# Optimization experiments

Measured on AMD Instinct MI355X. Metric: run time of the kernel, lower is better.

The kernel has to match this reference:

```python
import jax, jax.numpy as jnp
import numpy as np

B, D, UNITS = 32768, 1024, 1024
NB_FACTOR, SPARSITY = 3, 32
NB = D // SPARSITY  # 32 blocks of 32x32 per block-diagonal factor


def _block_t_matmul(kb, y):
    # kb: [nb, bi, bo] block-diagonal factor values; y: [nb*bi, batch]
    # computes blockdiag(kb)^T @ y without materializing the dense matrix
    nb, bi, bo = kb.shape
    yb = y.reshape(nb, bi, -1)                      # [nb, bi, batch]
    out = jnp.einsum('nio,nib->nob', kb, yb)        # [nb, bo, batch]
    return out.reshape(nb * bo, -1)


def setup_inputs() -> dict:
    key = jax.random.key(0)
    ks = jax.random.split(key, 9)
    return {
        'x': jax.random.normal(ks[0], (B, D), jnp.float32),
        'P0': jax.random.normal(ks[1], (D, D), jnp.float32),
        'P1': jax.random.normal(ks[2], (D, D), jnp.float32),
        'P2': jax.random.normal(ks[3], (D, D), jnp.float32),
        'P3': jax.random.normal(ks[4], (UNITS, UNITS), jnp.float32),
        'K0': jax.random.normal(ks[5], (NB, SPARSITY, SPARSITY), jnp.float32) * 0.05,
        'K1': jax.random.normal(ks[6], (NB, SPARSITY, SPARSITY), jnp.float32) * 0.05,
        'K2': jax.random.normal(ks[7], (NB, SPARSITY, SPARSITY), jnp.float32) * 0.05,
        'bias': jax.random.normal(ks[8], (UNITS,), jnp.float32),
    }


def reference(x, P0, P1, P2, P3, K0, K1, K2, bias):
    # output = (softmax(P3) @ Bd2^T @ softmax(P2) @ Bd1^T @ softmax(P1) @ Bd0^T @ softmax(P0) @ x^T)^T + bias
    y = x.T                                          # [D, B]
    y = jax.nn.softmax(P0, axis=1) @ y
    for kb, perm in ((K0, P1), (K1, P2), (K2, P3)):
        y = _block_t_matmul(kb, y)
        y = jax.nn.softmax(perm, axis=1) @ y
    out = y.T + bias                                 # [B, UNITS]
    return out
```

## Files before the change

kernel.cpp:

```cpp
#include <hip/hip_runtime.h>
#include <hip/hip_bf16.h>

typedef __bf16 bf16x8 __attribute__((ext_vector_type(8)));
typedef float f32x4 __attribute__((ext_vector_type(4)));
typedef unsigned short u16x8 __attribute__((ext_vector_type(8)));

__device__ __forceinline__ unsigned short f2bf(float f) {
  unsigned u = __float_as_uint(f);
  u += 0x7FFF + ((u >> 16) & 1);
  return (unsigned short)(u >> 16);
}
__device__ __forceinline__ float bf2f(unsigned short h) {
  return __uint_as_float((unsigned)h << 16);
}

__device__ __forceinline__ void gload_lds16(const void* g, void* l) {
  __builtin_amdgcn_global_load_lds(
      (const __attribute__((address_space(1))) void*)g,
      (__attribute__((address_space(3))) void*)l, 16, 0, 0);
}

__device__ __forceinline__ void convert_slice(const float* __restrict__ x,
                                              unsigned short* __restrict__ xb,
                                              int base8, int cnt8, int cb, int nb)
{
  int i = cb * 256 + (int)threadIdx.x;
  const int stride = nb * 256;
  for (; i < cnt8; i += stride) {
    const size_t g = (size_t)(base8 + i);
    float4 v0 = ((const float4*)x)[2 * g];
    float4 v1 = ((const float4*)x)[2 * g + 1];
    u16x8 uv;
    uv[0] = f2bf(v0.x); uv[1] = f2bf(v0.y); uv[2] = f2bf(v0.z); uv[3] = f2bf(v0.w);
    uv[4] = f2bf(v1.x); uv[5] = f2bf(v1.y); uv[6] = f2bf(v1.z); uv[7] = f2bf(v1.w);
    ((u16x8*)xb)[g] = uv;
  }
}

__global__ __launch_bounds__(256)
void softmax4_kernel(const float* __restrict__ P0, const float* __restrict__ P1,
                     const float* __restrict__ P2, const float* __restrict__ P3,
                     unsigned short* __restrict__ S,
                     const float* __restrict__ cvx, unsigned short* __restrict__ cvxb,
                     int cvt_cnt)
{
  if (blockIdx.x >= 4096) {
    convert_slice(cvx, cvxb, 0, cvt_cnt, blockIdx.x - 4096, gridDim.x - 4096);
    return;
  }
  const int bid = blockIdx.x;
  const int mat = bid >> 10, row = bid & 1023;
  const float* P = (mat == 0 ? P0 : mat == 1 ? P1 : mat == 2 ? P2 : P3) + (size_t)row * 1024;
  unsigned short* out = S + ((size_t)mat << 20) + (size_t)row * 1024;
  const int t = threadIdx.x, w = t >> 6, l = t & 63;
  float4 v = ((const float4*)P)[t];
  float mx = fmaxf(fmaxf(v.x, v.y), fmaxf(v.z, v.w));
  #pragma unroll
  for (int off = 32; off > 0; off >>= 1) mx = fmaxf(mx, __shfl_xor(mx, off));
  __shared__ float redA[4], redB[4];
  if (l == 0) redA[w] = mx;
  __syncthreads();
  mx = fmaxf(fmaxf(redA[0], redA[1]), fmaxf(redA[2], redA[3]));
  float e0 = __expf(v.x - mx), e1 = __expf(v.y - mx);
  float e2 = __expf(v.z - mx), e3 = __expf(v.w - mx);
  float s = e0 + e1 + e2 + e3;
  #pragma unroll
  for (int off = 32; off > 0; off >>= 1) s += __shfl_xor(s, off);
  if (l == 0) redB[w] = s;
  __syncthreads();
  s = redB[0] + redB[1] + redB[2] + redB[3];
  float inv = 1.0f / s;
  ushort4 o;
  o.x = f2bf(e0 * inv); o.y = f2bf(e1 * inv);
  o.z = f2bf(e2 * inv); o.w = f2bf(e3 * inv);
  ((ushort4*)out)[t] = o;
}

__device__ __forceinline__ void bdT_body(const float* __restrict__ Kb,
                                         const unsigned short* __restrict__ in,
                                         unsigned short* __restrict__ outT, int bid)
{
  const int n = bid >> 2;
  const int c = (bid & 3) * 256 + threadIdx.x;
  __shared__ float Ks[32][33];
  for (int t = threadIdx.x; t < 1024; t += 256)
    Ks[t >> 5][t & 31] = Kb[n * 1024 + t];
  __syncthreads();
  float ri[32];
  #pragma unroll
  for (int i = 0; i < 32; ++i)
    ri[i] = bf2f(in[(size_t)(n * 32 + i) * 1024 + c]);
  unsigned short ov[32];
  #pragma unroll
  for (int o = 0; o < 32; ++o) {
    float acc = 0.f;
    #pragma unroll
    for (int i = 0; i < 32; ++i) acc = fmaf(Ks[i][o], ri[i], acc);
    ov[o] = f2bf(acc);
  }
  u16x8* dst = (u16x8*)(outT + (size_t)c * 1024 + n * 32);
  const u16x8* src = (const u16x8*)ov;
  #pragma unroll
  for (int q = 0; q < 4; ++q) dst[q] = src[q];
}

__global__ __launch_bounds__(256)
void blockdiagT_dual_kernel(const float* Ka, const unsigned short* ina, unsigned short* outa,
                            const float* Kb2, const unsigned short* inb, unsigned short* outb,
                            const float* cvx, unsigned short* cvxb, int cvt_base, int cvt_cnt)
{
  const int bid = blockIdx.x;
  if (bid >= 256) {
    convert_slice(cvx, cvxb, cvt_base, cvt_cnt, bid - 256, gridDim.x - 256);
    return;
  }
  const bool sec = bid >= 128;
  bdT_body(sec ? Kb2 : Ka, sec ? inb : ina, sec ? outb : outa, sec ? bid - 128 : bid);
}

template<int TILE, bool A_FP32, bool OUT_BIAS, bool RBD>
__device__ __forceinline__ void gemm_body(const void* __restrict__ Av,
                                          const unsigned short* __restrict__ B,
                                          void* __restrict__ Cv, const float* __restrict__ bias,
                                          int N, int K, int nprim, int bid,
                                          const float* __restrict__ KR)
{
  constexpr int FR  = TILE / 32;
  constexpr int SIT = TILE / 32;
  __shared__ unsigned short Asm[TILE * 64];
  __shared__ unsigned short Bsm[TILE * 64];
  const int tid = threadIdx.x;
  const int w = tid >> 6, l = tid & 63;
  const int cpx = nprim >> 3;
  const int swz = (bid & 7) * cpx + (bid >> 3);
  const int ntn = N / TILE;
  const int n0 = (swz % ntn) * TILE;
  const int m0 = (swz / ntn) * TILE;
  const int wr = (w >> 1) * (TILE / 2), wc = (w & 1) * (TILE / 2);
  const int lr = l & 15, kg = (l >> 4) << 3;

  f32x4 acc[FR][FR] = {};
  const int KT = K >> 6;
  for (int kt = 0; kt < KT; ++kt) {
    const int k0 = kt << 6;
    if (kt) __syncthreads();
    #pragma unroll
    for (int it = 0; it < SIT; ++it) {
      int li = it * 256 + tid;
      int row = li >> 3, c8 = (li & 7) << 3;
      const unsigned short* g = B + (size_t)(n0 + row) * K + (k0 + c8);
      gload_lds16(g, (char*)Bsm + it * 4096 + w * 1024);
    }
    if (A_FP32) {
      const float* Af = (const float*)Av;
      #pragma unroll
      for (int p = 0; p < SIT; ++p) {
        int row = (tid >> 3) + p * 32;
        int c8 = (tid & 7) << 3;
        const float* g = Af + (size_t)(m0 + row) * K + (k0 + c8);
        float4 v0 = ((const float4*)g)[0];
        float4 v1 = ((const float4*)g)[1];
        u16x8 uv;
        uv[0] = f2bf(v0.x); uv[1] = f2bf(v0.y); uv[2] = f2bf(v0.z); uv[3] = f2bf(v0.w);
        uv[4] = f2bf(v1.x); uv[5] = f2bf(v1.y); uv[6] = f2bf(v1.z); uv[7] = f2bf(v1.w);
        *(u16x8*)&Asm[row * 64 + c8] = uv;
      }
    } else {
      const unsigned short* Ab = (const unsigned short*)Av;
      #pragma unroll
      for (int it = 0; it < SIT; ++it) {
        int li = it * 256 + tid;
        int row = li >> 3, c8 = (li & 7) << 3;
        const unsigned short* g = Ab + (size_t)(m0 + row) * K + (k0 + c8);
        gload_lds16(g, (char*)Asm + it * 4096 + w * 1024);
      }
    }
    __syncthreads();
    #pragma unroll
    for (int ks = 0; ks < 2; ++ks) {
      const int kb = ks * 32 + kg;
      bf16x8 af[FR], bfr[FR];
      #pragma unroll
      for (int i = 0; i < FR; ++i)
        af[i] = *(const bf16x8*)&Asm[(wr + i * 16 + lr) * 64 + kb];
      #pragma unroll
      for (int j = 0; j < FR; ++j)
        bfr[j] = *(const bf16x8*)&Bsm[(wc + j * 16 + lr) * 64 + kb];
      #pragma unroll
      for (int i = 0; i < FR; ++i)
        #pragma unroll
        for (int j = 0; j < FR; ++j)
          acc[i][j] = __builtin_amdgcn_mfma_f32_16x16x32_bf16(af[i], bfr[j], acc[i][j], 0, 0, 0);
    }
  }
  const int cr = (l >> 4) << 2;
  const int cc = l & 15;
  if (RBD) {
    __shared__ float tileS[64][65];
    __shared__ float Kt[2][32][33];
    __syncthreads();
    #pragma unroll
    for (int j = 0; j < FR; ++j)
      #pragma unroll
      for (int i = 0; i < FR; ++i)
        #pragma unroll
        for (int r = 0; r < 4; ++r)
          tileS[wr + i * 16 + cr + r][wc + j * 16 + cc] = acc[i][j][r];
    for (int idx = tid; idx < 2048; idx += 256) {
      int blk = idx >> 10, rem = idx & 1023;
      Kt[blk][rem >> 5][rem & 31] = KR[(size_t)((n0 >> 5) + blk) * 1024 + rem];
    }
    __syncthreads();
    const int row = tid & 63, cq = (tid >> 6) << 4;
    const int nb2 = cq >> 5, co = cq & 31;
    float av[16] = {};
    #pragma unroll 4
    for (int o = 0; o < 32; ++o) {
      float a = tileS[row][nb2 * 32 + o];
      #pragma unroll
      for (int ii = 0; ii < 16; ++ii)
        av[ii] = fmaf(a, Kt[nb2][o][co + ii], av[ii]);
    }
    u16x8 ov[2];
    #pragma unroll
    for (int ii = 0; ii < 16; ++ii) ov[ii >> 3][ii & 7] = f2bf(av[ii]);
    unsigned short* Cz = (unsigned short*)Cv;
    u16x8* dst = (u16x8*)&Cz[(size_t)(m0 + row) * N + n0 + cq];
    dst[0] = ov[0]; dst[1] = ov[1];
  } else if (OUT_BIAS) {
    float* C = (float*)Cv;
    #pragma unroll
    for (int j = 0; j < FR; ++j) {
      int col = n0 + wc + j * 16 + cc;
      float bv = bias[col];
      #pragma unroll
      for (int i = 0; i < FR; ++i) {
        int rbase = m0 + wr + i * 16 + cr;
        #pragma unroll
        for (int r = 0; r < 4; ++r)
          C[(size_t)(rbase + r) * N + col] = acc[i][j][r] + bv;
      }
    }
  } else {
    unsigned short* C = (unsigned short*)Cv;
    #pragma unroll
    for (int j = 0; j < FR; ++j) {
      int col = n0 + wc + j * 16 + cc;
      #pragma unroll
      for (int i = 0; i < FR; ++i) {
        int rbase = m0 + wr + i * 16 + cr;
        #pragma unroll
        for (int r = 0; r < 4; ++r)
          C[(size_t)(rbase + r) * N + col] = f2bf(acc[i][j][r]);
      }
    }
  }
}

template<int TILE, bool A_FP32, bool OUT_BIAS>
__global__ __launch_bounds__(256)
void gemm_bt_kernel(const void* __restrict__ Av, const unsigned short* __restrict__ B,
                    void* __restrict__ Cv, const float* __restrict__ bias,
                    int N, int K, int nprim,
                    const float* cvx, unsigned short* cvxb, int cvt_base, int cvt_cnt)
{
  if ((int)blockIdx.x >= nprim) {
    convert_slice(cvx, cvxb, cvt_base, cvt_cnt, blockIdx.x - nprim, gridDim.x - nprim);
    return;
  }
  gemm_body<TILE, A_FP32, OUT_BIAS, false>(Av, B, Cv, bias, N, K, nprim, blockIdx.x, nullptr);
}

__global__ __launch_bounds__(256)
void gemm_dual_kernel(const unsigned short* A0, const unsigned short* B0, unsigned short* C0,
                      const unsigned short* A1, const unsigned short* B1, unsigned short* C1,
                      const float* KR,
                      const float* cvx, unsigned short* cvxb, int cvt_base, int cvt_cnt)
{
  const int bid = blockIdx.x;
  if (bid >= 512) {
    convert_slice(cvx, cvxb, cvt_base, cvt_cnt, bid - 512, gridDim.x - 512);
    return;
  }
  if (bid < 256)
    gemm_body<64, false, false, false>(A0, B0, (void*)C0, nullptr, 1024, 1024, 256, bid, nullptr);
  else
    gemm_body<64, false, false, true>(A1, B1, (void*)C1, nullptr, 1024, 1024, 256, bid - 256, KR);
}

__global__ __launch_bounds__(512, 2)
void gemm256_kernel(const unsigned short* __restrict__ A,
                    const unsigned short* __restrict__ B,
                    float* __restrict__ C, const float* __restrict__ bias,
                    int N, int K)
{
  extern __shared__ __align__(16) char lds[];
  const int tid = threadIdx.x;
  const int w = tid >> 6, l = tid & 63;
  const int wm = w >> 2, wn = w & 3;
  const int lr = l & 15;
  const int klo = (l >> 4) << 4;
  const int sw  = (lr & 7) << 4;

  const int nwg = gridDim.x;
  const int bid = blockIdx.x;
  const int cpx = nwg >> 3;
  const int swz = (bid & 7) * cpx + (bid >> 3);
  const int ntn = N >> 8;
  const int n0 = (swz % ntn) << 8;
  const int m0 = (swz / ntn) << 8;

  unsigned int aoff[2][2], boff[2][2];
  #pragma unroll
  for (int q = 0; q < 2; ++q)
    #pragma unroll
    for (int it = 0; it < 2; ++it) {
      int L = it * 8192 + tid * 16;
      int r = L >> 7;
      int cs = (L & 127) ^ ((r & 7) << 4);
      aoff[q][it] = (unsigned)(m0 + q * 128 + r) * K + (cs >> 1);
      boff[q][it] = (unsigned)(n0 + q * 128 + r) * K + (cs >> 1);
    }
  char* ldsA = lds;
  char* ldsB = lds + 65536;
  const int wdst = w * 1024;

#define STG_A(bufo, q, k0) do { \
    gload_lds16(A + aoff[q][0] + (k0), ldsA + (bufo) + (q) * 16384 + wdst); \
    gload_lds16(A + aoff[q][1] + (k0), ldsA + (bufo) + (q) * 16384 + 8192 + wdst); } while (0)
#define STG_B(bufo, q, k0) do { \
    gload_lds16(B + boff[q][0] + (k0), ldsB + (bufo) + (q) * 16384 + wdst); \
    gload_lds16(B + boff[q][1] + (k0), ldsB + (bufo) + (q) * 16384 + 8192 + wdst); } while (0)

#define PH_RD(QI, QJ) \
    bf16x8 av0_[4], av1_[4], bv0_[2], bv1_[2]; \
    { const char* Ah = ldsA + b + (QI) * 16384; \
      const char* Bh = ldsB + b + (QJ) * 16384; \
      const int cb0 = klo ^ sw, cb1 = (64 + klo) ^ sw; \
      _Pragma("unroll") for (int i = 0; i < 4; ++i) { \
        av0_[i] = *(const bf16x8*)(Ah + (wm * 64 + i * 16 + lr) * 128 + cb0); \
        av1_[i] = *(const bf16x8*)(Ah + (wm * 64 + i * 16 + lr) * 128 + cb1); } \
      _Pragma("unroll") for (int j = 0; j < 2; ++j) { \
        bv0_[j] = *(const bf16x8*)(Bh + (wn * 32 + j * 16 + lr) * 128 + cb0); \
        bv1_[j] = *(const bf16x8*)(Bh + (wn * 32 + j * 16 + lr) * 128 + cb1); } }

#define PH_MM(QI, QJ) \
    __builtin_amdgcn_s_barrier(); \
    __builtin_amdgcn_s_setprio(1); \
    _Pragma("unroll") for (int i = 0; i < 4; ++i) \
      _Pragma("unroll") for (int j = 0; j < 2; ++j) { \
        acc[QI][QJ][i][j] = __builtin_amdgcn_mfma_f32_16x16x32_bf16(av0_[i], bv0_[j], acc[QI][QJ][i][j], 0, 0, 0); \
        acc[QI][QJ][i][j] = __builtin_amdgcn_mfma_f32_16x16x32_bf16(av1_[i], bv1_[j], acc[QI][QJ][i][j], 0, 0, 0); } \
    __builtin_amdgcn_s_setprio(0); \
    __builtin_amdgcn_s_barrier();

#define VM(n) asm volatile("s_waitcnt vmcnt(" #n ")" ::: "memory")

  f32x4 acc[2][2][4][2] = {};

  const int NT = K >> 6;
  STG_A(0, 0, 0);     STG_B(0, 0, 0);     STG_B(0, 1, 0);     STG_A(0, 1, 0);
  STG_A(32768, 0, 64); STG_B(32768, 0, 64); STG_B(32768, 1, 64); STG_A(32768, 1, 64);
  VM(0);
  __builtin_amdgcn_s_barrier();

  for (int t = 0; t < NT; ++t) {
    const int b  = (t & 1) ? 32768 : 0;
    const int nb = b ^ 32768;
    const int k1 = (t + 1) << 6;
    const int k2 = (t + 2) << 6;
    const bool sN1 = (t >= 1) && (t < NT - 1);
    const bool sN2 = (t < NT - 2);
    {
      PH_RD(0, 0);
      if (sN1) STG_B(nb, 1, k1);
      if (t == NT - 1) { VM(1); } else { VM(8); }
      PH_MM(0, 0);
    }
    {
      PH_RD(0, 1);
      if (sN1) STG_A(nb, 1, k1);
      if (t == NT - 1) { VM(0); } else { VM(8); }
      PH_MM(0, 1);
    }
    {
      PH_RD(1, 0);
      if (sN2) STG_A(b, 0, k2);
      if (t < NT - 1) { VM(8); }
      PH_MM(1, 0);
    }
    {
      PH_RD(1, 1);
      if (sN2) STG_B(b, 0, k2);
      if (t == NT - 2) { VM(4); } else if (t < NT - 2) { VM(8); }
      PH_MM(1, 1);
    }
  }

  const int cr = (l >> 4) << 2;
  const int cc = l & 15;
  #pragma unroll
  for (int qi = 0; qi < 2; ++qi)
    #pragma unroll
    for (int qj = 0; qj < 2; ++qj)
      #pragma unroll
      for (int j = 0; j < 2; ++j) {
        const int col = n0 + qj * 128 + wn * 32 + j * 16 + cc;
        const float bv = bias[col];
        #pragma unroll
        for (int i = 0; i < 4; ++i) {
          const int rbase = m0 + qi * 128 + wm * 64 + i * 16 + cr;
          #pragma unroll
          for (int r = 0; r < 4; ++r)
            C[(size_t)(rbase + r) * N + col] = acc[qi][qj][i][j][r] + bv;
        }
      }
#undef STG_A
#undef STG_B
#undef PH_RD
#undef PH_MM
#undef VM
}

extern "C" void kernel_launch(void* const* d_in, const int* in_sizes, int n_in,
                              void* d_out, int out_size, void* d_ws, size_t ws_size,
                              hipStream_t stream) {
  (void)in_sizes; (void)n_in; (void)out_size;
  const float* x    = (const float*)d_in[0];
  const float* P0   = (const float*)d_in[1];
  const float* P1   = (const float*)d_in[2];
  const float* P2   = (const float*)d_in[3];
  const float* P3   = (const float*)d_in[4];
  const float* K0   = (const float*)d_in[5];
  const float* K1   = (const float*)d_in[6];
  const float* K2   = (const float*)d_in[7];
  const float* bias = (const float*)d_in[8];

  unsigned short* S  = (unsigned short*)d_ws;
  unsigned short* s0 = S;
  unsigned short* s1 = S + (1u << 20);
  unsigned short* s2 = S + (2u << 20);
  unsigned short* s3 = S + (3u << 20);
  unsigned short* t0 = S + (4u << 20);
  unsigned short* t1 = S + (5u << 20);
  unsigned short* Xb = S + (6u << 20);
  const size_t need = ((size_t)6 * (1u << 20) + (size_t)32768 * 1024) * 2;
  const bool have_xb = ws_size >= need;
  unsigned short* xbp = have_xb ? Xb : nullptr;

  const int SL = 524288;
  const int cvt2 = have_xb ? 2 * SL : 0;
  const int tail_smx = have_xb ? 1024 : 0;
  const int tail_512 = have_xb ? 512 : 0;

  softmax4_kernel<<<4096 + tail_smx, 256, 0, stream>>>(P0, P1, P2, P3, S, x, xbp, cvt2);

  blockdiagT_dual_kernel<<<256 + tail_512, 256, 0, stream>>>(K2, s2, t0, K0, s0, t1,
                                                             x, xbp, 2 * SL, cvt2);

  gemm_dual_kernel<<<512 + tail_512, 256, 0, stream>>>(s3, t0, s0, t1, s1, t1, K1,
                                                       x, xbp, 4 * SL, cvt2);

  gemm_bt_kernel<64, false, false><<<256 + tail_512, 256, 0, stream>>>((const void*)s0, t1,
      (void*)t0, nullptr, 1024, 1024, 256, x, xbp, 6 * SL, cvt2);

  bool ok256 = false;
  if (have_xb) {
    hipError_t e = hipFuncSetAttribute((const void*)gemm256_kernel,
                                       hipFuncAttributeMaxDynamicSharedMemorySize, 131072);
    ok256 = (e == hipSuccess);
  }
  if (ok256) {
    gemm256_kernel<<<512, 512, 131072, stream>>>(Xb, t0, (float*)d_out, bias, 1024, 1024);
  } else if (have_xb) {
    gemm_bt_kernel<128, false, true><<<2048, 256, 0, stream>>>((const void*)Xb, t0,
        d_out, bias, 1024, 1024, 2048, nullptr, nullptr, 0, 0);
  } else {
    gemm_bt_kernel<128, true, true><<<2048, 256, 0, stream>>>((const void*)x, t0,
        d_out, bias, 1024, 1024, 2048, nullptr, nullptr, 0, 0);
  }
}
```

Baseline: 172.1 us.

## Replace 4-phase interleaved GEMM pipeline with simple double-buffered loop; reroute buffers

```diff
diff --git a/kernel.cpp b/kernel.cpp
--- a/kernel.cpp
+++ b/kernel.cpp
@@ -332,69 +332,51 @@
     gload_lds16(B + boff[q][0] + (k0), ldsB + (bufo) + (q) * 16384 + wdst); \
     gload_lds16(B + boff[q][1] + (k0), ldsB + (bufo) + (q) * 16384 + 8192 + wdst); } while (0)
 
-#define PH_RD(QI, QJ) \
-    bf16x8 av0_[4], av1_[4], bv0_[2], bv1_[2]; \
-    { const char* Ah = ldsA + b + (QI) * 16384; \
-      const char* Bh = ldsB + b + (QJ) * 16384; \
-      const int cb0 = klo ^ sw, cb1 = (64 + klo) ^ sw; \
-      _Pragma("unroll") for (int i = 0; i < 4; ++i) { \
-        av0_[i] = *(const bf16x8*)(Ah + (wm * 64 + i * 16 + lr) * 128 + cb0); \
-        av1_[i] = *(const bf16x8*)(Ah + (wm * 64 + i * 16 + lr) * 128 + cb1); } \
-      _Pragma("unroll") for (int j = 0; j < 2; ++j) { \
-        bv0_[j] = *(const bf16x8*)(Bh + (wn * 32 + j * 16 + lr) * 128 + cb0); \
-        bv1_[j] = *(const bf16x8*)(Bh + (wn * 32 + j * 16 + lr) * 128 + cb1); } }
-
-#define PH_MM(QI, QJ) \
-    __builtin_amdgcn_s_barrier(); \
-    __builtin_amdgcn_s_setprio(1); \
-    _Pragma("unroll") for (int i = 0; i < 4; ++i) \
-      _Pragma("unroll") for (int j = 0; j < 2; ++j) { \
-        acc[QI][QJ][i][j] = __builtin_amdgcn_mfma_f32_16x16x32_bf16(av0_[i], bv0_[j], acc[QI][QJ][i][j], 0, 0, 0); \
-        acc[QI][QJ][i][j] = __builtin_amdgcn_mfma_f32_16x16x32_bf16(av1_[i], bv1_[j], acc[QI][QJ][i][j], 0, 0, 0); } \
-    __builtin_amdgcn_s_setprio(0); \
+  f32x4 acc[2][2][4][2] = {};
+
+  STG_A(0, 0, 0); STG_B(0, 0, 0); STG_B(0, 1, 0); STG_A(0, 1, 0);
+
+  const int NT = K >> 6;
+  int curo = 0;
+  for (int t = 0; t < NT; ++t) {
+    const int nxto = curo ^ 32768;
+    const int k1 = (t + 1) << 6;
+    asm volatile("s_waitcnt vmcnt(0)" ::: "memory");
     __builtin_amdgcn_s_barrier();
-
-#define VM(n) asm volatile("s_waitcnt vmcnt(" #n ")" ::: "memory")
-
-  f32x4 acc[2][2][4][2] = {};
-
-  const int NT = K >> 6;
-  STG_A(0, 0, 0);     STG_B(0, 0, 0);     STG_B(0, 1, 0);     STG_A(0, 1, 0);
-  STG_A(32768, 0, 64); STG_B(32768, 0, 64); STG_B(32768, 1, 64); STG_A(32768, 1, 64);
-  VM(0);
-  __builtin_amdgcn_s_barrier();
-
-  for (int t = 0; t < NT; ++t) {
-    const int b  = (t & 1) ? 32768 : 0;
-    const int nb = b ^ 32768;
-    const int k1 = (t + 1) << 6;
-    const int k2 = (t + 2) << 6;
-    const bool sN1 = (t >= 1) && (t < NT - 1);
-    const bool sN2 = (t < NT - 2);
-    {
-      PH_RD(0, 0);
-      if (sN1) STG_B(nb, 1, k1);
-      if (t == NT - 1) { VM(1); } else { VM(8); }
-      PH_MM(0, 0);
-    }
-    {
-      PH_RD(0, 1);
-      if (sN1) STG_A(nb, 1, k1);
-      if (t == NT - 1) { VM(0); } else { VM(8); }
-      PH_MM(0, 1);
-    }
-    {
-      PH_RD(1, 0);
-      if (sN2) STG_A(b, 0, k2);
-      if (t < NT - 1) { VM(8); }
-      PH_MM(1, 0);
-    }
-    {
-      PH_RD(1, 1);
-      if (sN2) STG_B(b, 0, k2);
-      if (t == NT - 2) { VM(4); } else if (t < NT - 2) { VM(8); }
-      PH_MM(1, 1);
-    }
+    if (t + 1 < NT) { STG_A(nxto, 0, k1); STG_B(nxto, 0, k1); STG_B(nxto, 1, k1); STG_A(nxto, 1, k1); }
+    const char* Ab = ldsA + curo;
+    const char* Bb = ldsB + curo;
+    bf16x8 av[2][2][4];
+    bf16x8 bvr[2][2][2];
+    #pragma unroll
+    for (int ks = 0; ks < 2; ++ks) {
+      const int cb = (ks * 64 + klo) ^ sw;
+      #pragma unroll
+      for (int qi = 0; qi < 2; ++qi)
+        #pragma unroll
+        for (int i = 0; i < 4; ++i)
+          av[ks][qi][i] = *(const bf16x8*)(Ab + qi * 16384 + (wm * 64 + i * 16 + lr) * 128 + cb);
+      #pragma unroll
+      for (int qj = 0; qj < 2; ++qj)
+        #pragma unroll
+        for (int j = 0; j < 2; ++j)
+          bvr[ks][qj][j] = *(const bf16x8*)(Bb + qj * 16384 + (wn * 32 + j * 16 + lr) * 128 + cb);
+    }
+    __builtin_amdgcn_s_setprio(1);
+    #pragma unroll
+    for (int ks = 0; ks < 2; ++ks)
+      #pragma unroll
+      for (int qi = 0; qi < 2; ++qi)
+        #pragma unroll
+        for (int i = 0; i < 4; ++i)
+          #pragma unroll
+          for (int qj = 0; qj < 2; ++qj)
+            #pragma unroll
+            for (int j = 0; j < 2; ++j)
+              acc[qi][qj][i][j] = __builtin_amdgcn_mfma_f32_16x16x32_bf16(
+                  av[ks][qi][i], bvr[ks][qj][j], acc[qi][qj][i][j], 0, 0, 0);
+    __builtin_amdgcn_s_setprio(0);
+    curo = nxto;
   }
 
   const int cr = (l >> 4) << 2;
@@ -406,20 +388,17 @@
       #pragma unroll
       for (int j = 0; j < 2; ++j) {
         const int col = n0 + qj * 128 + wn * 32 + j * 16 + cc;
-        const float bv = bias[col];
+        const float bvv = bias[col];
         #pragma unroll
         for (int i = 0; i < 4; ++i) {
           const int rbase = m0 + qi * 128 + wm * 64 + i * 16 + cr;
           #pragma unroll
           for (int r = 0; r < 4; ++r)
-            C[(size_t)(rbase + r) * N + col] = acc[qi][qj][i][j][r] + bv;
+            C[(size_t)(rbase + r) * N + col] = acc[qi][qj][i][j][r] + bvv;
         }
       }
 #undef STG_A
 #undef STG_B
-#undef PH_RD
-#undef PH_MM
-#undef VM
 }
 
 extern "C" void kernel_launch(void* const* d_in, const int* in_sizes, int n_in,
@@ -458,10 +437,10 @@
   blockdiagT_dual_kernel<<<256 + tail_512, 256, 0, stream>>>(K2, s2, t0, K0, s0, t1,
                                                              x, xbp, 2 * SL, cvt2);
 
-  gemm_dual_kernel<<<512 + tail_512, 256, 0, stream>>>(s3, t0, s0, t1, s1, t1, K1,
+  gemm_dual_kernel<<<512 + tail_512, 256, 0, stream>>>(s3, t0, s0, t1, s1, s2, K1,
                                                        x, xbp, 4 * SL, cvt2);
 
-  gemm_bt_kernel<64, false, false><<<256 + tail_512, 256, 0, stream>>>((const void*)s0, t1,
+  gemm_bt_kernel<64, false, false><<<256 + tail_512, 256, 0, stream>>>((const void*)s0, s2,
       (void*)t0, nullptr, 1024, 1024, 256, x, xbp, 6 * SL, cvt2);
 
   bool ok256 = false;
```

Result: faster. 158.4 us, median of 3 (-8.0%).
